# Performance work log

Hardware: AMD Instinct MI355X
Metric: run time of the kernel (lower is better)

The kernel has to match this reference:

```python
import jax, jax.numpy as jnp
import numpy as np

N = 10000        # total nodes in batch
E = 320000       # total edges (before self-loops)
D_IN = 128       # node_dim
H_DIM = 64       # hidden_dim
HEADS = 4
B = 64           # number of graphs
NUM_EDGES = 1024 # actor output dim


def _lin(k, i, o):
    return jax.random.normal(k, (i, o), jnp.float32) / np.sqrt(i)


def setup_inputs() -> dict:
    key = jax.random.key(0)
    ks = jax.random.split(key, 32)
    x = jax.random.normal(ks[0], (N, D_IN), jnp.float32)
    edge_index = jax.random.randint(ks[1], (2, E), 0, N, dtype=jnp.int64)
    batch = jnp.sort(jax.random.randint(ks[2], (N,), 0, B, dtype=jnp.int64))
    inp = dict(x=x, edge_index=edge_index, batch=batch)
    # GAT layer 1: in=D_IN, heads=4, out=H_DIM, concat
    inp['W1'] = _lin(ks[3], D_IN, HEADS * H_DIM)
    inp['as1'] = jax.random.normal(ks[4], (HEADS, H_DIM), jnp.float32) * 0.1
    inp['ad1'] = jax.random.normal(ks[5], (HEADS, H_DIM), jnp.float32) * 0.1
    inp['b1'] = jnp.zeros((HEADS * H_DIM,), jnp.float32)
    # GAT layer 2: in=4*H_DIM, heads=4, out=H_DIM, concat
    inp['W2'] = _lin(ks[6], HEADS * H_DIM, HEADS * H_DIM)
    inp['as2'] = jax.random.normal(ks[7], (HEADS, H_DIM), jnp.float32) * 0.1
    inp['ad2'] = jax.random.normal(ks[8], (HEADS, H_DIM), jnp.float32) * 0.1
    inp['b2'] = jnp.zeros((HEADS * H_DIM,), jnp.float32)
    # GAT layer 3: in=4*H_DIM, heads=1, out=H_DIM, mean (concat=False)
    inp['W3'] = _lin(ks[9], HEADS * H_DIM, H_DIM)
    inp['as3'] = jax.random.normal(ks[10], (1, H_DIM), jnp.float32) * 0.1
    inp['ad3'] = jax.random.normal(ks[11], (1, H_DIM), jnp.float32) * 0.1
    inp['b3'] = jnp.zeros((H_DIM,), jnp.float32)
    # actor MLP
    inp['Wa1'] = _lin(ks[12], H_DIM, H_DIM); inp['ba1'] = jnp.zeros((H_DIM,), jnp.float32)
    inp['Wa2'] = _lin(ks[13], H_DIM, NUM_EDGES); inp['ba2'] = jnp.zeros((NUM_EDGES,), jnp.float32)
    # critic MLP
    inp['Wc1'] = _lin(ks[14], H_DIM, H_DIM); inp['bc1'] = jnp.zeros((H_DIM,), jnp.float32)
    inp['Wc2'] = _lin(ks[15], H_DIM, 1); inp['bc2'] = jnp.zeros((1,), jnp.float32)
    return inp


def gat_layer(x, src, dst, W, a_src, a_dst, bias, heads, out_dim, concat):
    # PyG GATConv: linear -> edge attention -> per-dst softmax -> scatter-add
    n = x.shape[0]
    h = (x @ W).reshape(n, heads, out_dim)            # [N,H,D]
    s = (h * a_src).sum(-1)                           # [N,H] attention src term
    d = (h * a_dst).sum(-1)                           # [N,H]
    e = jax.nn.leaky_relu(s[src] + d[dst], 0.2)       # [Eall,H]
    m = jax.ops.segment_max(e, dst, num_segments=n)   # stable softmax per dst node
    w = jnp.exp(e - m[dst])
    alpha = w / jax.ops.segment_sum(w, dst, num_segments=n)[dst]
    agg = jax.ops.segment_sum(h[src] * alpha[..., None], dst, num_segments=n)  # [N,H,D]
    o = agg.reshape(n, heads * out_dim) if concat else agg.mean(axis=1)
    return o + bias


def forward(x, edge_index, batch, W1, as1, ad1, b1, W2, as2, ad2, b2,
            W3, as3, ad3, b3, Wa1, ba1, Wa2, ba2, Wc1, bc1, Wc2, bc2):
    n = x.shape[0]
    loop = jnp.arange(n, dtype=edge_index.dtype)
    src = jnp.concatenate([edge_index[0], loop])      # add_self_loops=True (PyG default)
    dst = jnp.concatenate([edge_index[1], loop])
    h = jax.nn.relu(gat_layer(x, src, dst, W1, as1, ad1, b1, HEADS, H_DIM, True))
    h = jax.nn.relu(gat_layer(h, src, dst, W2, as2, ad2, b2, HEADS, H_DIM, True))
    h = jax.nn.relu(gat_layer(h, src, dst, W3, as3, ad3, b3, 1, H_DIM, False))
    # global_mean_pool
    counts = jax.ops.segment_sum(jnp.ones((n,), h.dtype), batch, num_segments=B)
    pooled = jax.ops.segment_sum(h, batch, num_segments=B) / jnp.maximum(counts, 1.0)[:, None]
    # heads (dropout is identity at inference)
    action = jnp.tanh(jax.nn.relu(pooled @ Wa1 + ba1) @ Wa2 + ba2)
    value = jax.nn.relu(pooled @ Wc1 + bc1) @ Wc2 + bc2
    return action, value


def reference(x, edge_index, batch, W1, as1, ad1, b1, W2, as2, ad2, b2,
              W3, as3, ad3, b3, Wa1, ba1, Wa2, ba2, Wc1, bc1, Wc2, bc2):
    return forward(x, edge_index, batch, W1, as1, ad1, b1, W2, as2, ad2, b2,
                   W3, as3, ad3, b3, Wa1, ba1, Wa2, ba2, Wc1, bc1, Wc2, bc2)
```

## Files before the change

kernel.cpp:

```cpp
#include <hip/hip_runtime.h>
#include <hip/hip_bf16.h>

#define NN 10000
#define EE 320000
#define EALL (EE + NN)
#define BG 64
#define AOUT 1024
#define CAP 128

#define SCB ((EALL + 255) / 256)

typedef __hip_bfloat16 bf16;
typedef __attribute__((ext_vector_type(8))) short bf16x8;
typedef __attribute__((ext_vector_type(4))) float f32x4;

__device__ __forceinline__ unsigned short f2bf(float f) {
    bf16 h = __float2bfloat16(f);
    return *reinterpret_cast<unsigned short*>(&h);
}
__device__ __forceinline__ float bf2f(unsigned short u) {
    bf16 h;
    *reinterpret_cast<unsigned short*>(&h) = u;
    return __bfloat162float(h);
}
__device__ __forceinline__ int iread(const void* p, int fi, long long idx) {
    return fi ? ((const int*)p)[idx] : (int)((const long long*)p)[idx];
}
__device__ __forceinline__ float fread1(const void* p, int ff, int idx) {
    return ff ? ((const float*)p)[idx] : bf2f(((const unsigned short*)p)[idx]);
}

struct WPtrs { const void* p[20]; };
#define CVT_TOT (1728 + 32768 + 65536 + 16384 + NN)
__global__ __launch_bounds__(256) void k_cvt_all(WPtrs wp, const void* __restrict__ xsrc,
                          float* __restrict__ wfv,
                          unsigned short* __restrict__ w1t, unsigned short* __restrict__ w2t,
                          unsigned short* __restrict__ w3t, int* __restrict__ cnt, int ffh) {
    __shared__ int sff;
    int ff = ffh;
    if (ffh < 0) {
        const int t = threadIdx.x;
        bool nanp = false;
        const uint4* xs4 = (const uint4*)xsrc;
        uint4 a = xs4[t * 8 + 0], b = xs4[t * 8 + 4];
        const unsigned int wds[8] = {a.x, a.y, a.z, a.w, b.x, b.y, b.z, b.w};
#pragma unroll
        for (int k = 0; k < 8; k++) {
            unsigned int w2 = wds[k];
            if ((w2 & 0x7F80u) == 0x7F80u || ((w2 >> 16) & 0x7F80u) == 0x7F80u) nanp = true;
        }
        unsigned long long bn = __ballot(nanp);
        if (t == 0) sff = 0;
        __syncthreads();
        if ((t & 63) == 0 && bn) atomicOr(&sff, 1);
        __syncthreads();
        ff = sff;
    }

    int i = blockIdx.x * 256 + threadIdx.x;
    if (i < 1728) {
        const int vsz[9]  = {256,256,256,256,256,256,64,64,64};
        const int vwp[9]  = {1,2,3,5,6,7,9,10,11};
        const int voff[9] = {0,256,512,768,1024,1280,1536,1600,1664};
        int seg = 0, off = 0;
        while (i - off >= vsz[seg]) { off += vsz[seg]; seg++; }
        int k = i - off;
        wfv[voff[seg] + k] = fread1(wp.p[vwp[seg]], ff, k);
        return;
    }
    i -= 1728;
    if (i < 32768) {
        int k = i >> 8, c = i & 255;
        float v = fread1(wp.p[0], ff, i);
        w1t[c * 128 + k] = f2bf(v);
        return;
    }
    i -= 32768;
    if (i < 65536) {
        int k = i >> 8, c = i & 255;
        float v = fread1(wp.p[4], ff, i);
        w2t[c * 256 + k] = f2bf(v);
        return;
    }
    i -= 65536;
    if (i < 16384) {
        int k = i >> 6, c = i & 63;
        float v = fread1(wp.p[8], ff, i);
        w3t[c * 256 + k] = f2bf(v);
        return;
    }
    i -= 16384;
    if (i < NN) cnt[i] = 0;
}

__global__ __launch_bounds__(256) void k_fuse1(const void* __restrict__ eisrc,
                                               const void* __restrict__ xsrc,
                                               int ffh, int fih,
                                               int* __restrict__ cnt, int* __restrict__ ssrc,
                                               const unsigned short* __restrict__ WT16,
                                               const float* __restrict__ asf,
                                               const float* __restrict__ adf,
                                               unsigned short* __restrict__ C16,
                                               float* __restrict__ sb, float* __restrict__ db) {
    constexpr int LDW = 40;
    __shared__ alignas(16) char smem[10240];
    __shared__ int sff, sfi;
    const int t = threadIdx.x;
    int ff = ffh, fi = fih;
    if (ffh < 0 || fih < 0) {
        bool nanp = false, odd = false;
        const uint4* xs4 = (const uint4*)xsrc;
        uint4 a = xs4[t * 8 + 0], b = xs4[t * 8 + 4];
        const unsigned int wds[8] = {a.x, a.y, a.z, a.w, b.x, b.y, b.z, b.w};
#pragma unroll
        for (int k = 0; k < 8; k++) {
            unsigned int w2 = wds[k];
            if ((w2 & 0x7F80u) == 0x7F80u || ((w2 >> 16) & 0x7F80u) == 0x7F80u) nanp = true;
        }
        odd = ((const unsigned int*)eisrc)[2 * t + 1] != 0u;
        unsigned long long bn = __ballot(nanp);
        unsigned long long bo = __ballot(odd);
        if (t == 0) { sff = 0; sfi = 0; }
        __syncthreads();
        if ((t & 63) == 0) {
            if (bn) atomicOr(&sff, 1);
            if (bo) atomicOr(&sfi, 1);
        }
        __syncthreads();
        ff = (ffh >= 0) ? ffh : sff;
        fi = (fih >= 0) ? fih : sfi;
    }

    if (blockIdx.x < SCB) {
        int e = blockIdx.x * 256 + t;
        if (e < EALL) {
            int dst = (e < EE) ? iread(eisrc, fi, (long long)EE + e) : (e - EE);
            int src = (e < EE) ? iread(eisrc, fi, e) : dst;
            int pos = atomicAdd(&cnt[dst], 1);
            if (pos < CAP) ssrc[(size_t)dst * CAP + pos] = src;
        }
        return;
    }
    unsigned short* As = (unsigned short*)smem;
    unsigned short* Bs = As + 64 * LDW;
    constexpr int K = 128, M = 256, H = M / 64;
    const int u = blockIdx.x - SCB;
    const int bx = u % 157;
    const int hh = u / 157;
    const int row0 = bx * 64, col0 = hh * 64;
    const int wv = t >> 6, lane = t & 63;
    const int m = lane & 15, q = lane >> 4;
    const int srow = t >> 2, skoff = (t & 3) * 8;

    f32x4 acc[4] = {};
    for (int k0 = 0; k0 < K; k0 += 32) {
        {
            int grow = row0 + srow;
            uint4 av = make_uint4(0u, 0u, 0u, 0u);
            if (grow < NN) {
                if (ff) {
                    const float* xp = (const float*)xsrc + (size_t)grow * K + k0 + skoff;
                    float4 fa = *(const float4*)xp;
                    float4 fb = *(const float4*)(xp + 4);
                    union { unsigned short u16[8]; uint4 v; } pk;
                    pk.u16[0] = f2bf(fa.x); pk.u16[1] = f2bf(fa.y);
                    pk.u16[2] = f2bf(fa.z); pk.u16[3] = f2bf(fa.w);
                    pk.u16[4] = f2bf(fb.x); pk.u16[5] = f2bf(fb.y);
                    pk.u16[6] = f2bf(fb.z); pk.u16[7] = f2bf(fb.w);
                    av = pk.v;
                } else {
                    av = *(const uint4*)((const unsigned short*)xsrc + (size_t)grow * K + k0 + skoff);
                }
            }
            *(uint4*)&As[srow * LDW + skoff] = av;
            uint4 bv = *(const uint4*)&WT16[(size_t)(col0 + srow) * K + k0 + skoff];
            *(uint4*)&Bs[srow * LDW + skoff] = bv;
        }
        __syncthreads();
        bf16x8 af = *(const bf16x8*)&As[(16 * wv + m) * LDW + q * 8];
#pragma unroll
        for (int ct = 0; ct < 4; ct++) {
            bf16x8 bfv = *(const bf16x8*)&Bs[(16 * ct + m) * LDW + q * 8];
            acc[ct] = __builtin_amdgcn_mfma_f32_16x16x32_bf16(af, bfv, acc[ct], 0, 0, 0);
        }
        __syncthreads();
    }
    float asv[4], adv[4];
#pragma unroll
    for (int ct = 0; ct < 4; ct++) {
        asv[ct] = asf[hh * 64 + 16 * ct + m];
        adv[ct] = adf[hh * 64 + 16 * ct + m];
    }
#pragma unroll
    for (int reg = 0; reg < 4; reg++) {
        int row = row0 + 16 * wv + q * 4 + reg;
        float ps = 0.f, pd = 0.f;
        if (row < NN) {
#pragma unroll
            for (int ct = 0; ct < 4; ct++) {
                float v = acc[ct][reg];
                C16[(size_t)row * M + col0 + 16 * ct + m] = f2bf(v);
                ps += v * asv[ct];
                pd += v * adv[ct];
            }
        }
#pragma unroll
        for (int off = 1; off < 16; off <<= 1) {
            ps += __shfl_xor(ps, off);
            pd += __shfl_xor(pd, off);
        }
        if (m == 0 && row < NN) { sb[row * H + hh] = ps; db[row * H + hh] = pd; }
    }
}

template<int K, int M>
__global__ __launch_bounds__(256) void k_gemm(const unsigned short* __restrict__ A16,
                                              const unsigned short* __restrict__ WT16,
                                              const float* __restrict__ asf,
                                              const float* __restrict__ adf,
                                              unsigned short* __restrict__ C16,
                                              float* __restrict__ sb, float* __restrict__ db) {
    constexpr int BK = 32;
    constexpr int H = M / 64;
    constexpr int LDW = 40;
    __shared__ unsigned short As[64 * LDW];
    __shared__ unsigned short Bs[64 * LDW];
    const int row0 = blockIdx.x * 64;
    const int col0 = blockIdx.y * 64;
    const int hh = blockIdx.y;
    const int t = threadIdx.x;
    const int wv = t >> 6;
    const int lane = t & 63;
    const int m = lane & 15;
    const int q = lane >> 4;
    const int srow = t >> 2;
    const int skoff = (t & 3) * 8;

    f32x4 acc[4] = {};

    for (int k0 = 0; k0 < K; k0 += BK) {
        {
            int grow = row0 + srow;
            uint4 av = make_uint4(0u, 0u, 0u, 0u);
            if (grow < NN) av = *(const uint4*)&A16[(size_t)grow * K + k0 + skoff];
            *(uint4*)&As[srow * LDW + skoff] = av;
            uint4 bv = *(const uint4*)&WT16[(size_t)(col0 + srow) * K + k0 + skoff];
            *(uint4*)&Bs[srow * LDW + skoff] = bv;
        }
        __syncthreads();
        bf16x8 af = *(const bf16x8*)&As[(16 * wv + m) * LDW + q * 8];
#pragma unroll
        for (int ct = 0; ct < 4; ct++) {
            bf16x8 bfv = *(const bf16x8*)&Bs[(16 * ct + m) * LDW + q * 8];
            acc[ct] = __builtin_amdgcn_mfma_f32_16x16x32_bf16(af, bfv, acc[ct], 0, 0, 0);
        }
        __syncthreads();
    }

    float asv[4], adv[4];
#pragma unroll
    for (int ct = 0; ct < 4; ct++) {
        asv[ct] = asf[hh * 64 + 16 * ct + m];
        adv[ct] = adf[hh * 64 + 16 * ct + m];
    }
#pragma unroll
    for (int reg = 0; reg < 4; reg++) {
        int row = row0 + 16 * wv + q * 4 + reg;
        float ps = 0.f, pd = 0.f;
        if (row < NN) {
#pragma unroll
            for (int ct = 0; ct < 4; ct++) {
                float v = acc[ct][reg];
                C16[(size_t)row * M + col0 + 16 * ct + m] = f2bf(v);
                ps += v * asv[ct];
                pd += v * adv[ct];
            }
        }
#pragma unroll
        for (int off = 1; off < 16; off <<= 1) {
            ps += __shfl_xor(ps, off);
            pd += __shfl_xor(pd, off);
        }
        if (m == 0 && row < NN) { sb[row * H + hh] = ps; db[row * H + hh] = pd; }
    }
}

__global__ __launch_bounds__(512) void k_agg4(const unsigned short* __restrict__ hbuf16,
                                              const float* __restrict__ sb,
                                              const float* __restrict__ db,
                                              const int* __restrict__ cnt,
                                              const int* __restrict__ ssrc,
                                              const float* __restrict__ bias,
                                              unsigned short* __restrict__ out16) {
    const int n = blockIdx.x;
    const int tid = threadIdx.x;
    const int start = n * CAP;
    const int end = start + min(cnt[n], CAP);
    const int wv = tid >> 6, lane = tid & 63;
    const int cg = tid & 31;
    const int eg = tid >> 5;
    const int chh = cg >> 3;
    __shared__ float accbuf[16 * 256];
    __shared__ float sww[8][4];
    const float dn = db[n * 4 + chh];

    float wsum = 0.f;
    float acc[8] = {};
#pragma unroll 2
    for (int p = start + eg; p < end; p += 16) {
        int s = ssrc[p];
        float e = sb[s * 4 + chh] + dn;
        e = e > 0.f ? e : 0.2f * e;
        float w2 = __expf(e);
        wsum += w2;
        const bf16x8 v = *(const bf16x8*)&hbuf16[(size_t)s * 256 + cg * 8];
#pragma unroll
        for (int i = 0; i < 8; i++)
            acc[i] += w2 * bf2f((unsigned short)v[i]);
    }
    {
        float* ab = &accbuf[eg * 256 + cg * 8];
#pragma unroll
        for (int i = 0; i < 8; i++) ab[i] = acc[i];
    }
    wsum += __shfl_xor(wsum, 32);
    if (lane < 32 && (cg & 7) == 0) sww[wv][chh] = wsum;
    __syncthreads();

    if (tid < 256) {
        const int h2 = tid >> 6;
        float wsh = 0.f;
#pragma unroll
        for (int wq = 0; wq < 8; wq++) wsh += sww[wq][h2];
        float o = 0.f;
#pragma unroll
        for (int e8 = 0; e8 < 16; e8++) o += accbuf[e8 * 256 + tid];
        o = o / wsh + bias[tid];
        out16[(size_t)n * 256 + tid] = f2bf(fmaxf(o, 0.f));
    }
}

__global__ __launch_bounds__(256) void k_agg1w(const unsigned short* __restrict__ hbuf16,
                                               const float* __restrict__ sb,
                                               const float* __restrict__ db,
                                               const int* __restrict__ cnt,
                                               const int* __restrict__ ssrc,
                                               const float* __restrict__ bias,
                                               unsigned short* __restrict__ out16) {
    __shared__ float accb[4 * 512];
    const int tid = threadIdx.x;
    const int wv = tid >> 6, lane = tid & 63;
    const int eg = lane >> 3, cg = lane & 7;
    const int n = blockIdx.x * 4 + wv;
    if (n >= NN) return;
    const int start = n * CAP;
    const int end = start + min(cnt[n], CAP);
    const float dn = db[n];
    float wsum = 0.f;
    float acc[8] = {};
#pragma unroll 4
    for (int p = start + eg; p < end; p += 8) {
        int s = ssrc[p];
        float e = sb[s] + dn;
        e = e > 0.f ? e : 0.2f * e;
        float w2 = __expf(e);
        wsum += w2;
        const bf16x8 v = *(const bf16x8*)&hbuf16[(size_t)s * 64 + cg * 8];
#pragma unroll
        for (int i = 0; i < 8; i++)
            acc[i] += w2 * bf2f((unsigned short)v[i]);
    }
    {
        float* ab = &accb[wv * 512 + eg * 64 + cg * 8];
#pragma unroll
        for (int i = 0; i < 8; i++) ab[i] = acc[i];
    }
    wsum += __shfl_xor(wsum, 8);
    wsum += __shfl_xor(wsum, 16);
    wsum += __shfl_xor(wsum, 32);
    float o = 0.f;
#pragma unroll
    for (int e8 = 0; e8 < 8; e8++) o += accb[wv * 512 + e8 * 64 + lane];
    o = o / wsum + bias[lane];
    out16[(size_t)n * 64 + lane] = f2bf(fmaxf(o, 0.f));
}

__global__ __launch_bounds__(256) void k_final(const unsigned short* __restrict__ feat16,
                                               const void* __restrict__ bsrc,
                                               const void* __restrict__ eisrc,
                                               const void* __restrict__ xsrc,
                                               int ffh, int fih,
                                               const void* __restrict__ Wa1, const void* __restrict__ ba1,
                                               const void* __restrict__ Wa2, const void* __restrict__ ba2,
                                               const void* __restrict__ Wc1, const void* __restrict__ bc1,
                                               const void* __restrict__ Wc2, const void* __restrict__ bc2,
                                               float* __restrict__ out) {
    __shared__ float red[256];
    __shared__ float p[64];
    __shared__ float a[64], cc[64];
    __shared__ int sff, sfi;
    const int g = blockIdx.x, t = threadIdx.x;
    int ff = ffh, fi = fih;
    if (ffh < 0 || fih < 0) {
        bool nanp = false, odd = false;
        const uint4* xs4 = (const uint4*)xsrc;
        uint4 av = xs4[t * 8 + 0], bv = xs4[t * 8 + 4];
        const unsigned int wds[8] = {av.x, av.y, av.z, av.w, bv.x, bv.y, bv.z, bv.w};
#pragma unroll
        for (int k = 0; k < 8; k++) {
            unsigned int w2 = wds[k];
            if ((w2 & 0x7F80u) == 0x7F80u || ((w2 >> 16) & 0x7F80u) == 0x7F80u) nanp = true;
        }
        odd = ((const unsigned int*)eisrc)[2 * t + 1] != 0u;
        unsigned long long bn = __ballot(nanp);
        unsigned long long bo = __ballot(odd);
        if (t == 0) { sff = 0; sfi = 0; }
        __syncthreads();
        if ((t & 63) == 0) {
            if (bn) atomicOr(&sff, 1);
            if (bo) atomicOr(&sfi, 1);
        }
        __syncthreads();
        ff = (ffh >= 0) ? ffh : sff;
        fi = (fih >= 0) ? fih : sfi;
    }
    int s, e;
    {
        int lo = 0, hi = NN;
        while (lo < hi) { int mid = (lo + hi) >> 1; if (iread(bsrc, fi, mid) < g) lo = mid + 1; else hi = mid; }
        s = lo;
        lo = 0; hi = NN;
        while (lo < hi) { int mid = (lo + hi) >> 1; if (iread(bsrc, fi, mid) < g + 1) lo = mid + 1; else hi = mid; }
        e = lo;
    }
    const int d = t & 63, c = t >> 6;
    float acc = 0.f;
    for (int n = s + c; n < e; n += 4) acc += bf2f(feat16[(size_t)n * 64 + d]);
    red[t] = acc; __syncthreads();
    if (c == 0) p[d] = (red[d] + red[64 + d] + red[128 + d] + red[192 + d])
                       / fmaxf((float)(e - s), 1.f);
    __syncthreads();
    if (t < 128) {
        int j = t & 63;
        const void* W  = (t < 64) ? Wa1 : Wc1;
        const void* bb = (t < 64) ? ba1 : bc1;
        float h = 0.f;
        if (ff) {
            const float* Wf = (const float*)W;
#pragma unroll 8
            for (int k = 0; k < 64; k++) h += p[k] * Wf[k * 64 + j];
        } else {
            const unsigned short* Wh = (const unsigned short*)W;
#pragma unroll 8
            for (int k = 0; k < 64; k++) h += p[k] * bf2f(Wh[k * 64 + j]);
        }
        h = fmaxf(h + fread1(bb, ff, j), 0.f);
        if (t < 64) a[j] = h; else cc[j] = h;
    }
    __syncthreads();
    float o[4] = {0.f, 0.f, 0.f, 0.f};
    if (ff) {
        const float* Wf = (const float*)Wa2;
        for (int k = 0; k < 64; k++) {
            float ak = a[k];
#pragma unroll
            for (int q = 0; q < 4; q++) o[q] += ak * Wf[k * AOUT + t + 256 * q];
        }
    } else {
        const unsigned short* Wh = (const unsigned short*)Wa2;
        for (int k = 0; k < 64; k++) {
            float ak = a[k];
#pragma unroll
            for (int q = 0; q < 4; q++) o[q] += ak * bf2f(Wh[k * AOUT + t + 256 * q]);
        }
    }
#pragma unroll
    for (int q = 0; q < 4; q++)
        out[g * AOUT + t + 256 * q] = tanhf(o[q] + fread1(ba2, ff, t + 256 * q));
    if (t == 0) {
        float v = 0.f;
        for (int k = 0; k < 64; k++) v += cc[k] * fread1(Wc2, ff, k);
        out[BG * AOUT + g] = v + fread1(bc2, ff, 0);
    }
}

extern "C" void kernel_launch(void* const* d_in, const int* in_sizes, int n_in,
                              void* d_out, int out_size, void* d_ws, size_t ws_size,
                              hipStream_t stream) {
    float* out = (float*)d_out;

    char* w = (char*)d_ws;
    auto alloc = [&](size_t bytes) { void* p = (void*)w; w += (bytes + 255) & ~size_t(255); return p; };
    float* wfv     = (float*)alloc((size_t)1728 * 4);
    unsigned short* w1t    = (unsigned short*)alloc((size_t)32768 * 2);
    unsigned short* w2t    = (unsigned short*)alloc((size_t)65536 * 2);
    unsigned short* w3t    = (unsigned short*)alloc((size_t)16384 * 2);
    unsigned short* actA16 = (unsigned short*)alloc((size_t)NN * 256 * 2);
    unsigned short* actB16 = (unsigned short*)alloc((size_t)NN * 256 * 2);
    float* sb      = (float*)alloc((size_t)NN * 4 * 4);
    float* db      = (float*)alloc((size_t)NN * 4 * 4);
    int*   cnt     = (int*)alloc((size_t)NN * 4);
    int*   ssrc    = (int*)alloc((size_t)NN * CAP * 4);

    int ffh = -1, fih = -1;
    if (in_sizes && n_in >= 2) {
        long long xs = in_sizes[0];
        if (xs == (long long)NN * 128 * 4) ffh = 1;
        else if (xs == (long long)NN * 128 * 2) ffh = 0;
        long long es = in_sizes[1];
        if (es == (long long)2 * EE * 8) fih = 0;
        else if (es == (long long)2 * EE * 4) fih = 1;
    }

    WPtrs wp;
    for (int s = 0; s < 20; s++) wp.p[s] = d_in[3 + s];
    k_cvt_all<<<(CVT_TOT + 255) / 256, 256, 0, stream>>>(
        wp, d_in[0], wfv, w1t, w2t, w3t, cnt, ffh);

    const float *as1f = wfv + 0,   *ad1f = wfv + 256,  *b1f = wfv + 512;
    const float *as2f = wfv + 768, *ad2f = wfv + 1024, *b2f = wfv + 1280;
    const float *as3f = wfv + 1536,*ad3f = wfv + 1600, *b3f = wfv + 1664;

    k_fuse1<<<SCB + 628, 256, 0, stream>>>(d_in[1], d_in[0], ffh, fih, cnt, ssrc,
                                           w1t, as1f, ad1f, actA16, sb, db);

    k_agg4<<<NN, 512, 0, stream>>>(actA16, sb, db, cnt, ssrc, b1f, actB16);

    k_gemm<256, 256><<<dim3(157, 4), 256, 0, stream>>>(actB16, w2t, as2f, ad2f, actA16, sb, db);
    k_agg4<<<NN, 512, 0, stream>>>(actA16, sb, db, cnt, ssrc, b2f, actB16);

    k_gemm<256, 64><<<dim3(157, 1), 256, 0, stream>>>(actB16, w3t, as3f, ad3f, actA16, sb, db);
    k_agg1w<<<(NN + 3) / 4, 256, 0, stream>>>(actA16, sb, db, cnt, ssrc, b3f, actB16);

    k_final<<<BG, 256, 0, stream>>>(actB16, d_in[2], d_in[1], d_in[0], ffh, fih,
                                    d_in[15], d_in[16], d_in[17], d_in[18],
                                    d_in[19], d_in[20], d_in[21], d_in[22], out);
}
```

Before: 238.2 us.

## Unify GAT aggregation into templated kernel with fewer threads per node

Merges the 4-head and 1-head aggregation kernels into one templated kernel. The 4-head version now uses 256 threads per node (8 edge groups) instead of 512 (16 edge groups), each thread handling more edges with deeper unrolling. The 1-head version now launches one 64-thread block per node instead of packing four nodes per block. The aim is to cut shared-memory reduction and sync overhead and let more blocks reside per CU, at the cost of less edge-level parallelism per node and many small blocks for the last layer.

After: 225.1 us. 5.5% less time.

```diff
diff --git a/kernel.cpp b/kernel.cpp
--- a/kernel.cpp
+++ b/kernel.cpp
@@ -285,104 +285,71 @@
     }
 }
 
-__global__ __launch_bounds__(512) void k_agg4(const unsigned short* __restrict__ hbuf16,
-                                              const float* __restrict__ sb,
-                                              const float* __restrict__ db,
-                                              const int* __restrict__ cnt,
-                                              const int* __restrict__ ssrc,
-                                              const float* __restrict__ bias,
-                                              unsigned short* __restrict__ out16) {
+template<int H>
+__global__ void k_agg(const unsigned short* __restrict__ hbuf16, const float* __restrict__ sb,
+                      const float* __restrict__ db, const int* __restrict__ cnt,
+                      const int* __restrict__ ssrc, const float* __restrict__ bias,
+                      unsigned short* __restrict__ out16) {
+    constexpr int M = H * 64;
+    constexpr int NW = M / 64;
+    constexpr int CG = M / 8;
+    constexpr int LCG = (H == 4) ? 5 : 3;
     const int n = blockIdx.x;
     const int tid = threadIdx.x;
     const int start = n * CAP;
     const int end = start + min(cnt[n], CAP);
-    const int wv = tid >> 6, lane = tid & 63;
-    const int cg = tid & 31;
-    const int eg = tid >> 5;
-    const int chh = cg >> 3;
-    __shared__ float accbuf[16 * 256];
-    __shared__ float sww[8][4];
-    const float dn = db[n * 4 + chh];
-
-    float wsum = 0.f;
-    float acc[8] = {};
-#pragma unroll 2
-    for (int p = start + eg; p < end; p += 16) {
-        int s = ssrc[p];
-        float e = sb[s * 4 + chh] + dn;
-        e = e > 0.f ? e : 0.2f * e;
-        float w2 = __expf(e);
-        wsum += w2;
-        const bf16x8 v = *(const bf16x8*)&hbuf16[(size_t)s * 256 + cg * 8];
-#pragma unroll
-        for (int i = 0; i < 8; i++)
-            acc[i] += w2 * bf2f((unsigned short)v[i]);
-    }
-    {
-        float* ab = &accbuf[eg * 256 + cg * 8];
-#pragma unroll
-        for (int i = 0; i < 8; i++) ab[i] = acc[i];
-    }
-    wsum += __shfl_xor(wsum, 32);
-    if (lane < 32 && (cg & 7) == 0) sww[wv][chh] = wsum;
-    __syncthreads();
-
-    if (tid < 256) {
-        const int h2 = tid >> 6;
-        float wsh = 0.f;
-#pragma unroll
-        for (int wq = 0; wq < 8; wq++) wsh += sww[wq][h2];
-        float o = 0.f;
-#pragma unroll
-        for (int e8 = 0; e8 < 16; e8++) o += accbuf[e8 * 256 + tid];
-        o = o / wsh + bias[tid];
-        out16[(size_t)n * 256 + tid] = f2bf(fmaxf(o, 0.f));
-    }
-}
-
-__global__ __launch_bounds__(256) void k_agg1w(const unsigned short* __restrict__ hbuf16,
-                                               const float* __restrict__ sb,
-                                               const float* __restrict__ db,
-                                               const int* __restrict__ cnt,
-                                               const int* __restrict__ ssrc,
-                                               const float* __restrict__ bias,
-                                               unsigned short* __restrict__ out16) {
-    __shared__ float accb[4 * 512];
-    const int tid = threadIdx.x;
-    const int wv = tid >> 6, lane = tid & 63;
-    const int eg = lane >> 3, cg = lane & 7;
-    const int n = blockIdx.x * 4 + wv;
-    if (n >= NN) return;
-    const int start = n * CAP;
-    const int end = start + min(cnt[n], CAP);
-    const float dn = db[n];
+    const int wv = tid >> 6;
+    const int lane = tid & 63;
+    const int cg = tid & (CG - 1);
+    const int eg = tid >> LCG;
+    const int chh = (H == 4) ? (cg >> 3) : 0;
+    __shared__ float accbuf[8 * M];
+    __shared__ float sww[NW][H];
+    const float dn = db[n * H + chh];
+
     float wsum = 0.f;
     float acc[8] = {};
 #pragma unroll 4
     for (int p = start + eg; p < end; p += 8) {
         int s = ssrc[p];
-        float e = sb[s] + dn;
+        float e = sb[s * H + chh] + dn;
         e = e > 0.f ? e : 0.2f * e;
         float w2 = __expf(e);
         wsum += w2;
-        const bf16x8 v = *(const bf16x8*)&hbuf16[(size_t)s * 64 + cg * 8];
+        const bf16x8 v = *(const bf16x8*)&hbuf16[(size_t)s * M + cg * 8];
 #pragma unroll
         for (int i = 0; i < 8; i++)
             acc[i] += w2 * bf2f((unsigned short)v[i]);
     }
+
     {
-        float* ab = &accb[wv * 512 + eg * 64 + cg * 8];
+        float* ab = &accbuf[eg * M + cg * 8];
 #pragma unroll
         for (int i = 0; i < 8; i++) ab[i] = acc[i];
     }
-    wsum += __shfl_xor(wsum, 8);
-    wsum += __shfl_xor(wsum, 16);
-    wsum += __shfl_xor(wsum, 32);
+    if constexpr (NW > 1) {
+        wsum += __shfl_xor(wsum, 32);
+        if (lane < 32 && (cg & 7) == 0) sww[wv][chh] = wsum;
+    } else {
+        wsum += __shfl_xor(wsum, 8);
+        wsum += __shfl_xor(wsum, 16);
+        wsum += __shfl_xor(wsum, 32);
+    }
+    __syncthreads();
+
+    float wsh;
+    if constexpr (NW > 1) {
+        const int h2 = tid >> 6;
+        wsh = sww[0][h2] + sww[1][h2] + sww[2][h2] + sww[3][h2];
+    } else {
+        wsh = wsum;
+    }
+
     float o = 0.f;
 #pragma unroll
-    for (int e8 = 0; e8 < 8; e8++) o += accb[wv * 512 + e8 * 64 + lane];
-    o = o / wsum + bias[lane];
-    out16[(size_t)n * 64 + lane] = f2bf(fmaxf(o, 0.f));
+    for (int e8 = 0; e8 < 8; e8++) o += accbuf[e8 * M + tid];
+    o = o / wsh + bias[tid];
+    out16[(size_t)n * M + tid] = f2bf(fmaxf(o, 0.f));
 }
 
 __global__ __launch_bounds__(256) void k_final(const unsigned short* __restrict__ feat16,
@@ -524,13 +491,13 @@
     k_fuse1<<<SCB + 628, 256, 0, stream>>>(d_in[1], d_in[0], ffh, fih, cnt, ssrc,
                                            w1t, as1f, ad1f, actA16, sb, db);
 
-    k_agg4<<<NN, 512, 0, stream>>>(actA16, sb, db, cnt, ssrc, b1f, actB16);
+    k_agg<4><<<NN, 256, 0, stream>>>(actA16, sb, db, cnt, ssrc, b1f, actB16);
 
     k_gemm<256, 256><<<dim3(157, 4), 256, 0, stream>>>(actB16, w2t, as2f, ad2f, actA16, sb, db);
-    k_agg4<<<NN, 512, 0, stream>>>(actA16, sb, db, cnt, ssrc, b2f, actB16);
+    k_agg<4><<<NN, 256, 0, stream>>>(actA16, sb, db, cnt, ssrc, b2f, actB16);
 
     k_gemm<256, 64><<<dim3(157, 1), 256, 0, stream>>>(actB16, w3t, as3f, ad3f, actA16, sb, db);
-    k_agg1w<<<(NN + 3) / 4, 256, 0, stream>>>(actA16, sb, db, cnt, ssrc, b3f, actB16);
+    k_agg<1><<<NN, 64, 0, stream>>>(actA16, sb, db, cnt, ssrc, b3f, actB16);
 
     k_final<<<BG, 256, 0, stream>>>(actB16, d_in[2], d_in[1], d_in[0], ffh, fih,
                                     d_in[15], d_in[16], d_in[17], d_in[18],
```

## Split 4-head aggregation into two half-blocks per node and use one-wave layer-3 aggregation

Applied to the files above, without the earlier changes.

The 512-thread per-node aggregation kernel is replaced by 128-thread blocks that each handle two of the four heads, launched twice per node (2*NN blocks). Each block uses a smaller shared reduction buffer and loops over edges with 8 edge groups instead of 16. The layer-3 aggregation moves from four nodes per 256-thread block to one node per 64-thread block. The aim is smaller blocks with less shared memory and cheaper reductions, giving better occupancy and load balance. In exchange, edge indices and attention logits are loaded twice per node, and many more blocks are launched.

Result: faster. 225.7 us (-5.3%).

```diff
diff --git a/kernel.cpp b/kernel.cpp
--- a/kernel.cpp
+++ b/kernel.cpp
@@ -285,77 +285,73 @@
     }
 }
 
-__global__ __launch_bounds__(512) void k_agg4(const unsigned short* __restrict__ hbuf16,
-                                              const float* __restrict__ sb,
-                                              const float* __restrict__ db,
-                                              const int* __restrict__ cnt,
-                                              const int* __restrict__ ssrc,
-                                              const float* __restrict__ bias,
-                                              unsigned short* __restrict__ out16) {
-    const int n = blockIdx.x;
-    const int tid = threadIdx.x;
-    const int start = n * CAP;
-    const int end = start + min(cnt[n], CAP);
-    const int wv = tid >> 6, lane = tid & 63;
-    const int cg = tid & 31;
-    const int eg = tid >> 5;
-    const int chh = cg >> 3;
-    __shared__ float accbuf[16 * 256];
-    __shared__ float sww[8][4];
-    const float dn = db[n * 4 + chh];
-
-    float wsum = 0.f;
-    float acc[8] = {};
-#pragma unroll 2
-    for (int p = start + eg; p < end; p += 16) {
-        int s = ssrc[p];
-        float e = sb[s * 4 + chh] + dn;
-        e = e > 0.f ? e : 0.2f * e;
-        float w2 = __expf(e);
-        wsum += w2;
-        const bf16x8 v = *(const bf16x8*)&hbuf16[(size_t)s * 256 + cg * 8];
-#pragma unroll
-        for (int i = 0; i < 8; i++)
-            acc[i] += w2 * bf2f((unsigned short)v[i]);
-    }
-    {
-        float* ab = &accbuf[eg * 256 + cg * 8];
-#pragma unroll
-        for (int i = 0; i < 8; i++) ab[i] = acc[i];
-    }
-    wsum += __shfl_xor(wsum, 32);
-    if (lane < 32 && (cg & 7) == 0) sww[wv][chh] = wsum;
-    __syncthreads();
-
-    if (tid < 256) {
-        const int h2 = tid >> 6;
-        float wsh = 0.f;
-#pragma unroll
-        for (int wq = 0; wq < 8; wq++) wsh += sww[wq][h2];
-        float o = 0.f;
-#pragma unroll
-        for (int e8 = 0; e8 < 16; e8++) o += accbuf[e8 * 256 + tid];
-        o = o / wsh + bias[tid];
-        out16[(size_t)n * 256 + tid] = f2bf(fmaxf(o, 0.f));
-    }
-}
-
-__global__ __launch_bounds__(256) void k_agg1w(const unsigned short* __restrict__ hbuf16,
+__global__ __launch_bounds__(128) void k_aggh4(const unsigned short* __restrict__ hbuf16,
                                                const float* __restrict__ sb,
                                                const float* __restrict__ db,
                                                const int* __restrict__ cnt,
                                                const int* __restrict__ ssrc,
                                                const float* __restrict__ bias,
                                                unsigned short* __restrict__ out16) {
-    __shared__ float accb[4 * 512];
+    const int bid = blockIdx.x;
+    const int n = (bid >= NN) ? bid - NN : bid;
+    const int ho = (bid >= NN) ? 2 : 0;
     const int tid = threadIdx.x;
-    const int wv = tid >> 6, lane = tid & 63;
-    const int eg = lane >> 3, cg = lane & 7;
-    const int n = blockIdx.x * 4 + wv;
-    if (n >= NN) return;
     const int start = n * CAP;
     const int end = start + min(cnt[n], CAP);
+    const int wv = tid >> 6, lane = tid & 63;
+    const int cg = tid & 15;
+    const int eg = tid >> 4;
+    const int chl = cg >> 3;
+    const int head = ho + chl;
+    __shared__ float accbuf[8 * 128];
+    __shared__ float sww[2][2];
+    const float dn = db[n * 4 + head];
+
+    float wsum = 0.f;
+    float acc[8] = {};
+#pragma unroll 4
+    for (int p = start + eg; p < end; p += 8) {
+        int s = ssrc[p];
+        float e = sb[s * 4 + head] + dn;
+        e = e > 0.f ? e : 0.2f * e;
+        float w2 = __expf(e);
+        wsum += w2;
+        const bf16x8 v = *(const bf16x8*)&hbuf16[(size_t)s * 256 + ho * 64 + cg * 8];
+#pragma unroll
+        for (int i = 0; i < 8; i++)
+            acc[i] += w2 * bf2f((unsigned short)v[i]);
+    }
+    {
+        float* ab = &accbuf[eg * 128 + cg * 8];
+#pragma unroll
+        for (int i = 0; i < 8; i++) ab[i] = acc[i];
+    }
+    wsum += __shfl_xor(wsum, 16);
+    wsum += __shfl_xor(wsum, 32);
+    if (lane < 16 && (cg & 7) == 0) sww[wv][chl] = wsum;
+    __syncthreads();
+    const int h2 = tid >> 6;
+    const float wsh = sww[0][h2] + sww[1][h2];
+    float o = 0.f;
+#pragma unroll
+    for (int e8 = 0; e8 < 8; e8++) o += accbuf[e8 * 128 + tid];
+    o = o / wsh + bias[ho * 64 + tid];
+    out16[(size_t)n * 256 + ho * 64 + tid] = f2bf(fmaxf(o, 0.f));
+}
+
+__global__ void k_agg1(const unsigned short* __restrict__ hbuf16, const float* __restrict__ sb,
+                       const float* __restrict__ db, const int* __restrict__ cnt,
+                       const int* __restrict__ ssrc, const float* __restrict__ bias,
+                       unsigned short* __restrict__ out16) {
+    const int n = blockIdx.x;
+    const int tid = threadIdx.x;
+    const int start = n * CAP;
+    const int end = start + min(cnt[n], CAP);
+    const int cg = tid & 7;
+    const int eg = tid >> 3;
+    __shared__ float accbuf[8 * 64];
     const float dn = db[n];
+
     float wsum = 0.f;
     float acc[8] = {};
 #pragma unroll 4
@@ -371,18 +367,20 @@
             acc[i] += w2 * bf2f((unsigned short)v[i]);
     }
     {
-        float* ab = &accb[wv * 512 + eg * 64 + cg * 8];
+        float* ab = &accbuf[eg * 64 + cg * 8];
 #pragma unroll
         for (int i = 0; i < 8; i++) ab[i] = acc[i];
     }
     wsum += __shfl_xor(wsum, 8);
     wsum += __shfl_xor(wsum, 16);
     wsum += __shfl_xor(wsum, 32);
+    __syncthreads();
+
     float o = 0.f;
 #pragma unroll
-    for (int e8 = 0; e8 < 8; e8++) o += accb[wv * 512 + e8 * 64 + lane];
-    o = o / wsum + bias[lane];
-    out16[(size_t)n * 64 + lane] = f2bf(fmaxf(o, 0.f));
+    for (int e8 = 0; e8 < 8; e8++) o += accbuf[e8 * 64 + tid];
+    o = o / wsum + bias[tid];
+    out16[(size_t)n * 64 + tid] = f2bf(fmaxf(o, 0.f));
 }
 
 __global__ __launch_bounds__(256) void k_final(const unsigned short* __restrict__ feat16,
@@ -524,13 +522,13 @@
     k_fuse1<<<SCB + 628, 256, 0, stream>>>(d_in[1], d_in[0], ffh, fih, cnt, ssrc,
                                            w1t, as1f, ad1f, actA16, sb, db);
 
-    k_agg4<<<NN, 512, 0, stream>>>(actA16, sb, db, cnt, ssrc, b1f, actB16);
+    k_aggh4<<<2 * NN, 128, 0, stream>>>(actA16, sb, db, cnt, ssrc, b1f, actB16);
 
     k_gemm<256, 256><<<dim3(157, 4), 256, 0, stream>>>(actB16, w2t, as2f, ad2f, actA16, sb, db);
-    k_agg4<<<NN, 512, 0, stream>>>(actA16, sb, db, cnt, ssrc, b2f, actB16);
+    k_aggh4<<<2 * NN, 128, 0, stream>>>(actA16, sb, db, cnt, ssrc, b2f, actB16);
 
     k_gemm<256, 64><<<dim3(157, 1), 256, 0, stream>>>(actB16, w3t, as3f, ad3f, actA16, sb, db);
-    k_agg1w<<<(NN + 3) / 4, 256, 0, stream>>>(actA16, sb, db, cnt, ssrc, b3f, actB16);
+    k_agg1<<<NN, 64, 0, stream>>>(actA16, sb, db, cnt, ssrc, b3f, actB16);
 
     k_final<<<BG, 256, 0, stream>>>(actB16, d_in[2], d_in[1], d_in[0], ffh, fih,
                                     d_in[15], d_in[16], d_in[17], d_in[18],
```
